# Kernel tuning notes

Hardware: AMD Instinct MI355X
Metric: run time of the kernel (lower is better)

## Reference

```python
import jax, jax.numpy as jnp
import numpy as np

BN_EPS = 1e-5


def setup_inputs() -> dict:
    key = jax.random.key(0)
    ks = jax.random.split(key, 10)
    N, C, T, V, S, IC = 128, 64, 288, 16, 3, 16
    x = jax.random.normal(ks[0], (N, C, T, V), dtype=jnp.float32)
    A_base = jax.random.uniform(ks[1], (S, V, V), dtype=jnp.float32)
    PA = jax.random.normal(ks[2], (S, V, V), dtype=jnp.float32) * 1e-3
    Wa = jax.random.normal(ks[3], (S, IC, C), dtype=jnp.float32) * 0.1
    ba = jax.random.normal(ks[4], (S, IC), dtype=jnp.float32) * 0.1
    Wb = jax.random.normal(ks[5], (S, IC, C), dtype=jnp.float32) * 0.1
    bb = jax.random.normal(ks[6], (S, IC), dtype=jnp.float32) * 0.1
    Wd = jax.random.normal(ks[7], (S, C, C), dtype=jnp.float32) * 0.1
    bd = jax.random.normal(ks[8], (S, C), dtype=jnp.float32) * 0.1
    gamma = jnp.ones((C,), dtype=jnp.float32)
    beta = jnp.zeros((C,), dtype=jnp.float32)
    return {"x": x, "A_base": A_base, "PA": PA, "Wa": Wa, "ba": ba,
            "Wb": Wb, "bb": bb, "Wd": Wd, "bd": bd,
            "gamma": gamma, "beta": beta}


def reference(x, A_base, PA, Wa, ba, Wb, bb, Wd, bd, gamma, beta):
    N, C, T, V = x.shape
    S, IC, _ = Wa.shape
    A = A_base + PA  # [s,v,w]
    # 1x1 convs for all subsets at once: [n,s,ic,t,v]
    fa = jnp.einsum('nctv,sic->nsitv', x, Wa) + ba[None, :, :, None, None]
    fb = jnp.einsum('nctv,sic->nsitv', x, Wb) + bb[None, :, :, None, None]
    # A1: permute(0,3,1,2).view(N,V,IC*T) -> [n,s,v,(ic*t)]
    A1 = fa.transpose(0, 1, 4, 2, 3).reshape(N, S, V, IC * T)
    # A2: view(N, IC*T, V) -> [n,s,(ic*t),v]
    A2 = fb.reshape(N, S, IC * T, V)
    att = jnp.einsum('nsvk,nskw->nsvw', A1, A2) / float(IC * T)
    att = jax.nn.softmax(att, axis=2)  # torch softmax(dim=1) on [N,V,V]
    att = att + A[None]  # [n,s,v,w]
    # x.view(N,C*T,V) @ att, per subset: [n,s,c,t,w]
    z = jnp.einsum('nctv,nsvw->nsctw', x, att)
    # conv_d per subset then sum over subsets
    y = jnp.einsum('nsctw,soc->notw', z, Wd) + bd.sum(0)[None, :, None, None]
    # inference BN (running mean 0, var 1)
    scale = gamma / jnp.sqrt(1.0 + BN_EPS)
    y = y * scale[None, :, None, None] + beta[None, :, None, None]
    # residual (in_channels == out_channels -> identity down path)
    return y + x
```

## Files before the change

### kernel.cpp

```cpp
#include <hip/hip_runtime.h>
#include <math.h>

#define NN 128
#define CC 64
#define TT 288
#define VV 16
#define SS 3
#define ICC 16

#define SLICES 6
#define TSL (TT / SLICES)
#define CHUNKS (TSL / 8)

typedef __attribute__((ext_vector_type(8))) short s16x8;
typedef __attribute__((ext_vector_type(4))) float f32x4;

#define MFMA16(a, b, c) __builtin_amdgcn_mfma_f32_16x16x32_bf16(a, b, c, 0, 0, 0)

__device__ __forceinline__ unsigned short f2bf(float f) {
    union { float f; unsigned u; } x; x.f = f;
    unsigned r = (x.u + 0x7FFFu + ((x.u >> 16) & 1u)) >> 16;
    return (unsigned short)r;
}

__device__ __forceinline__ unsigned cvt2bf(float lo, float hi) {
    unsigned r;
    asm("v_cvt_pk_bf16_f32 %0, %1, %2" : "=v"(r) : "v"(lo), "v"(hi));
    return r;
}

__device__ __forceinline__ s16x8 zero8() {
    s16x8 z;
#pragma unroll
    for (int j = 0; j < 8; ++j) z[j] = 0;
    return z;
}

__device__ __forceinline__ s16x8 cvt8g(const float* p) {
    float4 a = *(const float4*)p;
    float4 b = *(const float4*)(p + 4);
    union { unsigned u[4]; s16x8 v; } r;
    r.u[0] = cvt2bf(a.x, a.y); r.u[1] = cvt2bf(a.z, a.w);
    r.u[2] = cvt2bf(b.x, b.y); r.u[3] = cvt2bf(b.z, b.w);
    return r.v;
}

__global__ void k_prep(const float* __restrict__ bd, const float* __restrict__ gamma,
                       const float* __restrict__ beta, const float* __restrict__ Wd,
                       float* __restrict__ cmul, float* __restrict__ cadd,
                       unsigned short* __restrict__ wd_bf) {
    const int tid = threadIdx.x;
    if (blockIdx.x == 0 && tid < CC) {
        float mul = gamma[tid] * rsqrtf(1.0f + 1e-5f);
        float add = (bd[tid] + bd[CC + tid] + bd[2 * CC + tid]) * mul + beta[tid];
        cmul[tid] = mul;
        cadd[tid] = add;
    }
    for (int e = blockIdx.x * 256 + tid; e < SS * CC * CC; e += 16 * 256)
        wd_bf[e] = f2bf(Wd[e]);
}

__global__ __launch_bounds__(256) void k_logits(
    const float* __restrict__ x,
    const float* __restrict__ Wa, const float* __restrict__ ba,
    const float* __restrict__ Wb, const float* __restrict__ bb,
    float* __restrict__ part)
{
    const int b    = blockIdx.x;
    const int n    = b / SLICES;
    const int sl   = b % SLICES;
    const int tid  = threadIdx.x;
    const int lane = tid & 63;
    const int wave = tid >> 6;
    const int q    = lane >> 4;
    const int m    = lane & 15;

    __shared__ __align__(16) unsigned short fa_l[SS][16][136];
    __shared__ __align__(16) unsigned short fb_l[SS][16][136];
    __shared__ float red[SS][4][256];

    s16x8 wa[SS][2], wb[SS][2];
    float4 ba_r[SS], bb_r[SS];
#pragma unroll
    for (int s = 0; s < SS; ++s) {
#pragma unroll
        for (int kt = 0; kt < 2; ++kt) {
            wa[s][kt] = cvt8g(Wa + ((size_t)(s * ICC + m) * CC + kt * 32 + q * 8));
            wb[s][kt] = cvt8g(Wb + ((size_t)(s * ICC + m) * CC + kt * 32 + q * 8));
        }
        ba_r[s] = *(const float4*)(ba + s * ICC + q * 4);
        bb_r[s] = *(const float4*)(bb + s * ICC + q * 4);
    }

    f32x4 accL[SS];
#pragma unroll
    for (int s = 0; s < SS; ++s)
#pragma unroll
        for (int r = 0; r < 4; ++r) accL[s][r] = 0.0f;

    const float* xn = x + (size_t)n * CC * TT * VV;
    const int tw = sl * TSL + wave * 2;

    for (int ch = 0; ch < CHUNKS; ++ch) {
        s16x8 bx[2][2];
#pragma unroll
        for (int tli = 0; tli < 2; ++tli) {
            const float* pt = xn + (size_t)(tw + ch * 8 + tli) * VV + m;
#pragma unroll
            for (int kt = 0; kt < 2; ++kt) {
                const float* p = pt + (size_t)(kt * 32 + q * 8) * (TT * VV);
                float f0 = p[0 * TT * VV], f1 = p[1 * TT * VV];
                float f2 = p[2 * TT * VV], f3 = p[3 * TT * VV];
                float f4 = p[4 * TT * VV], f5 = p[5 * TT * VV];
                float f6 = p[6 * TT * VV], f7 = p[7 * TT * VV];
                union { unsigned u[4]; s16x8 v; } r;
                r.u[0] = cvt2bf(f0, f1); r.u[1] = cvt2bf(f2, f3);
                r.u[2] = cvt2bf(f4, f5); r.u[3] = cvt2bf(f6, f7);
                bx[tli][kt] = r.v;
            }
        }

#pragma unroll
        for (int s = 0; s < SS; ++s) {
#pragma unroll
            for (int tli = 0; tli < 2; ++tli) {
                const int tl = wave * 2 + tli;
                f32x4 aa, ab;
                aa[0] = ba_r[s].x; aa[1] = ba_r[s].y; aa[2] = ba_r[s].z; aa[3] = ba_r[s].w;
                ab[0] = bb_r[s].x; ab[1] = bb_r[s].y; ab[2] = bb_r[s].z; ab[3] = bb_r[s].w;
#pragma unroll
                for (int kt = 0; kt < 2; ++kt) {
                    aa = MFMA16(wa[s][kt], bx[tli][kt], aa);
                    ab = MFMA16(wb[s][kt], bx[tli][kt], ab);
                }
                uint2 ua, ub;
                ua.x = cvt2bf(aa[0], aa[1]); ua.y = cvt2bf(aa[2], aa[3]);
                ub.x = cvt2bf(ab[0], ab[1]); ub.y = cvt2bf(ab[2], ab[3]);
                *reinterpret_cast<uint2*>(&fa_l[s][m][tl * 16 + 4 * q]) = ua;
                *reinterpret_cast<uint2*>(&fb_l[s][m][tl * 16 + 4 * q]) = ub;
            }
            s16x8 A2 = *(const s16x8*)&fa_l[s][m][wave * 32 + q * 8];
            s16x8 B2 = *(const s16x8*)&fb_l[s][m][wave * 32 + q * 8];
            accL[s] = MFMA16(A2, B2, accL[s]);
        }
    }

    __syncthreads();
#pragma unroll
    for (int s = 0; s < SS; ++s)
#pragma unroll
        for (int r = 0; r < 4; ++r)
            red[s][wave][(4 * q + r) * 16 + m] = accL[s][r];
    __syncthreads();
#pragma unroll
    for (int s = 0; s < SS; ++s) {
        float v = red[s][0][tid & 255] + red[s][1][tid & 255] +
                  red[s][2][tid & 255] + red[s][3][tid & 255];
        part[((size_t)(sl * NN + n) * SS + s) * 256 + tid] = v;
    }
}

__global__ __launch_bounds__(256) void k_softmax(
    const float* __restrict__ part,
    const float* __restrict__ A_base, const float* __restrict__ PA,
    float* __restrict__ att)
{
    const int n = blockIdx.x / SS;
    const int s = blockIdx.x % SS;
    const int tid = threadIdx.x;
    const int w = tid & 15;

    __shared__ float l[256];
    size_t base = ((size_t)n * SS + s) * 256;
    float mine = 0.0f;
#pragma unroll
    for (int p = 0; p < SLICES; ++p)
        mine += part[(size_t)p * (NN * SS * 256) + base + tid];
    mine *= (1.0f / (ICC * TT));
    l[tid] = mine;
    __syncthreads();

    float mx = -1e30f;
#pragma unroll
    for (int v2 = 0; v2 < 16; ++v2) mx = fmaxf(mx, l[v2 * 16 + w]);
    float sm = 0.f;
#pragma unroll
    for (int v2 = 0; v2 < 16; ++v2) sm += __expf(l[v2 * 16 + w] - mx);
    float r = __expf(mine - mx) / sm;

    int aidx = (s * VV * VV) + tid;
    att[base + tid] = r + A_base[aidx] + PA[aidx];
}

__global__ __launch_bounds__(256) void k_out(
    const float* __restrict__ x, const float* __restrict__ att,
    const unsigned short* __restrict__ wd_bf,
    const float* __restrict__ cmul, const float* __restrict__ cadd,
    float* __restrict__ out)
{
    const int b  = blockIdx.x;
    const int n  = b / (TT / 8);
    const int t0 = (b % (TT / 8)) * 8;

    const int tid  = threadIdx.x;
    const int lane = tid & 63;
    const int wave = tid >> 6;
    const int q    = lane >> 4;
    const int m    = lane & 15;

    __shared__ __align__(16) unsigned short zs[4][32][72];
    __shared__ __align__(16) unsigned short attL[SS][16][24];

    for (int e = tid; e < SS * 256; e += 256) {
        int ss = e >> 8, vv = (e >> 4) & 15, ww = e & 15;
        attL[ss][ww][vv] = f2bf(att[((size_t)n * SS + ss) * 256 + vv * 16 + ww]);
    }

    s16x8 xf[4][2];
#pragma unroll
    for (int cc = 0; cc < 4; ++cc)
#pragma unroll
        for (int u = 0; u < 2; ++u) {
            s16x8 f = zero8();
            if (q < 2) {
                const float* p = x + ((size_t)(n * CC + cc * 16 + m) * TT +
                                      (t0 + wave * 2 + u)) * VV + q * 8;
                f = cvt8g(p);
            }
            xf[cc][u] = f;
        }

    __syncthreads();

    f32x4 acc[4][2];
#pragma unroll
    for (int p = 0; p < 4; ++p)
#pragma unroll
        for (int u = 0; u < 2; ++u)
#pragma unroll
            for (int r = 0; r < 4; ++r) acc[p][u][r] = 0.0f;

#pragma unroll
    for (int s = 0; s < SS; ++s) {
        s16x8 af = zero8();
        if (q < 2) af = *(const s16x8*)&attL[s][m][q * 8];

#pragma unroll
        for (int u = 0; u < 2; ++u)
#pragma unroll
            for (int cc = 0; cc < 4; ++cc) {
                f32x4 z;
#pragma unroll
                for (int r = 0; r < 4; ++r) z[r] = 0.0f;
                z = MFMA16(xf[cc][u], af, z);
                uint2 uz;
                uz.x = cvt2bf(z[0], z[1]); uz.y = cvt2bf(z[2], z[3]);
                *reinterpret_cast<uint2*>(&zs[wave][u * 16 + m][cc * 16 + 4 * q]) = uz;
            }

        s16x8 zf[2][2];
#pragma unroll
        for (int u = 0; u < 2; ++u)
#pragma unroll
            for (int kt = 0; kt < 2; ++kt)
                zf[u][kt] = *(const s16x8*)&zs[wave][u * 16 + m][kt * 32 + q * 8];

#pragma unroll
        for (int p = 0; p < 4; ++p) {
            s16x8 wf[2];
#pragma unroll
            for (int kt = 0; kt < 2; ++kt)
                wf[kt] = *(const s16x8*)(wd_bf +
                           ((size_t)(s * CC + p * 16 + m) * CC + kt * 32 + q * 8));
#pragma unroll
            for (int u = 0; u < 2; ++u)
#pragma unroll
                for (int kt = 0; kt < 2; ++kt)
                    acc[p][u] = MFMA16(wf[kt], zf[u][kt], acc[p][u]);
        }
    }

#pragma unroll
    for (int p = 0; p < 4; ++p) {
        float4 mu = *(const float4*)(cmul + p * 16 + 4 * q);
        float4 ad = *(const float4*)(cadd + p * 16 + 4 * q);
        float mur[4] = {mu.x, mu.y, mu.z, mu.w};
        float adr[4] = {ad.x, ad.y, ad.z, ad.w};
#pragma unroll
        for (int u = 0; u < 2; ++u) {
            int t = t0 + wave * 2 + u;
#pragma unroll
            for (int r = 0; r < 4; ++r) {
                int o = p * 16 + 4 * q + r;
                size_t gi = ((size_t)(n * CC + o) * TT + t) * VV + m;
                out[gi] = acc[p][u][r] * mur[r] + adr[r] + x[gi];
            }
        }
    }
}

extern "C" void kernel_launch(void* const* d_in, const int* in_sizes, int n_in,
                              void* d_out, int out_size, void* d_ws, size_t ws_size,
                              hipStream_t stream) {
    const float* x      = (const float*)d_in[0];
    const float* A_base = (const float*)d_in[1];
    const float* PA     = (const float*)d_in[2];
    const float* Wa     = (const float*)d_in[3];
    const float* ba     = (const float*)d_in[4];
    const float* Wb     = (const float*)d_in[5];
    const float* bb     = (const float*)d_in[6];
    const float* Wd     = (const float*)d_in[7];
    const float* bd     = (const float*)d_in[8];
    const float* gamma  = (const float*)d_in[9];
    const float* beta   = (const float*)d_in[10];
    float* out = (float*)d_out;

    float* part = (float*)d_ws;
    float* att  = part;
    float* cmul = part + (size_t)SLICES * NN * SS * 256;
    float* cadd = cmul + CC;
    unsigned short* wd_bf = (unsigned short*)(cadd + CC);

    k_prep<<<16, 256, 0, stream>>>(bd, gamma, beta, Wd, cmul, cadd, wd_bf);
    k_logits<<<NN * SLICES, 256, 0, stream>>>(x, Wa, ba, Wb, bb, part);
    k_softmax<<<NN * SS, 256, 0, stream>>>(part, A_base, PA, att);
    k_out<<<NN * (TT / 8), 256, 0, stream>>>(x, att, wd_bf, cmul, cadd, out);
}
```

Baseline: 417.4 us.

## Stage x and Wd through swizzled LDS with coalesced loads and stores

In the logits kernel, x is loaded as coalesced float4 rows into a register prefetch buffer, converted to bf16 and written to an XOR-swizzled LDS tile. MFMA fragments are then read from that tile, replacing the per-lane strided gathers, and the next chunk is prefetched while the current one computes. The time slices per sample double. The output kernel now handles 16 timesteps per block. It stages x and the bf16 Wd weights in swizzled LDS and routes results through LDS so the residual add and stores use coalesced float4 accesses. This raises LDS use and adds barriers in exchange for fewer uncoalesced global transactions.

After: 340.9 us. 1.22x faster.

```diff
diff --git a/kernel.cpp b/kernel.cpp
--- a/kernel.cpp
+++ b/kernel.cpp
@@ -8,9 +8,11 @@
 #define SS 3
 #define ICC 16
 
-#define SLICES 6
+#define SLICES 12
 #define TSL (TT / SLICES)
 #define CHUNKS (TSL / 8)
+
+#define OTB 16
 
 typedef __attribute__((ext_vector_type(8))) short s16x8;
 typedef __attribute__((ext_vector_type(4))) float f32x4;
@@ -43,6 +45,15 @@
     r.u[0] = cvt2bf(a.x, a.y); r.u[1] = cvt2bf(a.z, a.w);
     r.u[2] = cvt2bf(b.x, b.y); r.u[3] = cvt2bf(b.z, b.w);
     return r.v;
+}
+
+__device__ __forceinline__ int xaddr(int col, int c) {
+    int chunk = ((c >> 3) ^ (col & 7) ^ ((col >> 3) & 7)) & 7;
+    return col * 64 + chunk * 8 + (c & 7);
+}
+__device__ __forceinline__ int xaddr16(int col, int ck) {
+    int chunk = (ck ^ (col & 7) ^ ((col >> 3) & 7)) & 7;
+    return col * 64 + chunk * 8;
 }
 
 __global__ void k_prep(const float* __restrict__ bd, const float* __restrict__ gamma,
@@ -75,9 +86,9 @@
     const int q    = lane >> 4;
     const int m    = lane & 15;
 
+    __shared__ __align__(16) unsigned short xsb[128 * 64];
     __shared__ __align__(16) unsigned short fa_l[SS][16][136];
     __shared__ __align__(16) unsigned short fb_l[SS][16][136];
-    __shared__ float red[SS][4][256];
 
     s16x8 wa[SS][2], wb[SS][2];
     float4 ba_r[SS], bb_r[SS];
@@ -99,24 +110,48 @@
         for (int r = 0; r < 4; ++r) accL[s][r] = 0.0f;
 
     const float* xn = x + (size_t)n * CC * TT * VV;
-    const int tw = sl * TSL + wave * 2;
-
+    const int tbase = sl * TSL;
+
+    float4 px[8];
+#pragma unroll
+    for (int i = 0; i < 8; ++i) {
+        int f4 = tid + i * 256;
+        int c = f4 >> 5, col4 = (f4 & 31) * 4;
+        px[i] = *(const float4*)(xn + (size_t)c * (TT * VV) + (size_t)tbase * VV + col4);
+    }
+
+#pragma unroll
     for (int ch = 0; ch < CHUNKS; ++ch) {
+        __syncthreads();
+#pragma unroll
+        for (int i = 0; i < 8; ++i) {
+            int f4 = tid + i * 256;
+            int c = f4 >> 5, col4 = (f4 & 31) * 4;
+            unsigned s01 = cvt2bf(px[i].x, px[i].y);
+            unsigned s23 = cvt2bf(px[i].z, px[i].w);
+            xsb[xaddr(col4 + 0, c)] = (unsigned short)(s01 & 0xffff);
+            xsb[xaddr(col4 + 1, c)] = (unsigned short)(s01 >> 16);
+            xsb[xaddr(col4 + 2, c)] = (unsigned short)(s23 & 0xffff);
+            xsb[xaddr(col4 + 3, c)] = (unsigned short)(s23 >> 16);
+        }
+        __syncthreads();
+
         s16x8 bx[2][2];
 #pragma unroll
         for (int tli = 0; tli < 2; ++tli) {
-            const float* pt = xn + (size_t)(tw + ch * 8 + tli) * VV + m;
-#pragma unroll
-            for (int kt = 0; kt < 2; ++kt) {
-                const float* p = pt + (size_t)(kt * 32 + q * 8) * (TT * VV);
-                float f0 = p[0 * TT * VV], f1 = p[1 * TT * VV];
-                float f2 = p[2 * TT * VV], f3 = p[3 * TT * VV];
-                float f4 = p[4 * TT * VV], f5 = p[5 * TT * VV];
-                float f6 = p[6 * TT * VV], f7 = p[7 * TT * VV];
-                union { unsigned u[4]; s16x8 v; } r;
-                r.u[0] = cvt2bf(f0, f1); r.u[1] = cvt2bf(f2, f3);
-                r.u[2] = cvt2bf(f4, f5); r.u[3] = cvt2bf(f6, f7);
-                bx[tli][kt] = r.v;
+            int col = (wave * 2 + tli) * 16 + m;
+#pragma unroll
+            for (int kt = 0; kt < 2; ++kt)
+                bx[tli][kt] = *(const s16x8*)&xsb[xaddr16(col, kt * 4 + q)];
+        }
+
+        if (ch + 1 < CHUNKS) {
+#pragma unroll
+            for (int i = 0; i < 8; ++i) {
+                int f4 = tid + i * 256;
+                int c = f4 >> 5, col4 = (f4 & 31) * 4;
+                px[i] = *(const float4*)(xn + (size_t)c * (TT * VV) +
+                                         (size_t)(tbase + (ch + 1) * 8) * VV + col4);
             }
         }
 
@@ -146,16 +181,17 @@
     }
 
     __syncthreads();
+    float* red = (float*)xsb;
 #pragma unroll
     for (int s = 0; s < SS; ++s)
 #pragma unroll
         for (int r = 0; r < 4; ++r)
-            red[s][wave][(4 * q + r) * 16 + m] = accL[s][r];
+            red[(s * 4 + wave) * 256 + (4 * q + r) * 16 + m] = accL[s][r];
     __syncthreads();
 #pragma unroll
     for (int s = 0; s < SS; ++s) {
-        float v = red[s][0][tid & 255] + red[s][1][tid & 255] +
-                  red[s][2][tid & 255] + red[s][3][tid & 255];
+        float v = red[(s * 4 + 0) * 256 + tid] + red[(s * 4 + 1) * 256 + tid] +
+                  red[(s * 4 + 2) * 256 + tid] + red[(s * 4 + 3) * 256 + tid];
         part[((size_t)(sl * NN + n) * SS + s) * 256 + tid] = v;
     }
 }
@@ -199,8 +235,8 @@
     float* __restrict__ out)
 {
     const int b  = blockIdx.x;
-    const int n  = b / (TT / 8);
-    const int t0 = (b % (TT / 8)) * 8;
+    const int n  = b / (TT / OTB);
+    const int t0 = (b % (TT / OTB)) * OTB;
 
     const int tid  = threadIdx.x;
     const int lane = tid & 63;
@@ -208,35 +244,64 @@
     const int q    = lane >> 4;
     const int m    = lane & 15;
 
-    __shared__ __align__(16) unsigned short zs[4][32][72];
+    __shared__ __align__(16) unsigned char uni[36864];
+    __shared__ __align__(16) unsigned short wdl[SS * 64 * 64];
     __shared__ __align__(16) unsigned short attL[SS][16][24];
 
+    unsigned short* xsb = (unsigned short*)uni;
+    unsigned short* zsb = (unsigned short*)uni;
+    float*          osb = (float*)uni;
+
+    {
+        const float* xrow0 = x + ((size_t)(n * CC) * TT + t0) * VV;
+#pragma unroll
+        for (int i = 0; i < 16; ++i) {
+            int c = wave * 16 + i;
+            float4 f = *(const float4*)(xrow0 + (size_t)c * (TT * VV) + lane * 4);
+            uint2 u2; u2.x = cvt2bf(f.x, f.y); u2.y = cvt2bf(f.z, f.w);
+            int tcol  = lane * 4;
+            int chunk = (tcol >> 3) ^ (c & 7);
+            *(uint2*)&xsb[c * 256 + chunk * 8 + (tcol & 7)] = u2;
+        }
+    }
+#pragma unroll
+    for (int i = 0; i < 12; ++i) {
+        int g  = tid + i * 256;
+        int s  = g >> 10;
+        int r1 = g & 1023;
+        int o  = r1 >> 4, c4 = r1 & 15;
+        uint2 w2 = *(const uint2*)(wd_bf + ((size_t)(s * 64 + o) * 64 + c4 * 4));
+        int chunk = (c4 >> 1) ^ (o & 7);
+        *(uint2*)&wdl[(s * 64 + o) * 64 + chunk * 8 + (c4 & 1) * 4] = w2;
+    }
     for (int e = tid; e < SS * 256; e += 256) {
         int ss = e >> 8, vv = (e >> 4) & 15, ww = e & 15;
         attL[ss][ww][vv] = f2bf(att[((size_t)n * SS + ss) * 256 + vv * 16 + ww]);
     }
 
-    s16x8 xf[4][2];
+    __syncthreads();
+
+    s16x8 xf[4][4];
 #pragma unroll
     for (int cc = 0; cc < 4; ++cc)
 #pragma unroll
-        for (int u = 0; u < 2; ++u) {
+        for (int u = 0; u < 4; ++u) {
             s16x8 f = zero8();
             if (q < 2) {
-                const float* p = x + ((size_t)(n * CC + cc * 16 + m) * TT +
-                                      (t0 + wave * 2 + u)) * VV + q * 8;
-                f = cvt8g(p);
+                int c = cc * 16 + m;
+                int chunk = ((4 * wave + u) * 2 + q) ^ (c & 7);
+                f = *(const s16x8*)&xsb[c * 256 + chunk * 8];
             }
             xf[cc][u] = f;
         }
 
     __syncthreads();
 
-    f32x4 acc[4][2];
+    f32x4 acc[4][4];
 #pragma unroll
     for (int p = 0; p < 4; ++p)
 #pragma unroll
-        for (int u = 0; u < 2; ++u)
+        for (int u = 0; u < 4; ++u)
 #pragma unroll
             for (int r = 0; r < 4; ++r) acc[p][u][r] = 0.0f;
 
@@ -246,34 +311,36 @@
         if (q < 2) af = *(const s16x8*)&attL[s][m][q * 8];
 
 #pragma unroll
-        for (int u = 0; u < 2; ++u)
+        for (int u = 0; u < 4; ++u)
 #pragma unroll
             for (int cc = 0; cc < 4; ++cc) {
                 f32x4 z;
 #pragma unroll
                 for (int r = 0; r < 4; ++r) z[r] = 0.0f;
                 z = MFMA16(xf[cc][u], af, z);
-                uint2 uz;
-                uz.x = cvt2bf(z[0], z[1]); uz.y = cvt2bf(z[2], z[3]);
-                *reinterpret_cast<uint2*>(&zs[wave][u * 16 + m][cc * 16 + 4 * q]) = uz;
+                uint2 uz; uz.x = cvt2bf(z[0], z[1]); uz.y = cvt2bf(z[2], z[3]);
+                *(uint2*)&zsb[((wave * 64) + u * 16 + m) * 72 + cc * 16 + 4 * q] = uz;
             }
 
-        s16x8 zf[2][2];
-#pragma unroll
-        for (int u = 0; u < 2; ++u)
+        s16x8 zf[4][2];
+#pragma unroll
+        for (int u = 0; u < 4; ++u)
 #pragma unroll
             for (int kt = 0; kt < 2; ++kt)
-                zf[u][kt] = *(const s16x8*)&zs[wave][u * 16 + m][kt * 32 + q * 8];
+                zf[u][kt] = *(const s16x8*)&zsb[((wave * 64) + u * 16 + m) * 72 +
+                                                kt * 32 + q * 8];
 
 #pragma unroll
         for (int p = 0; p < 4; ++p) {
             s16x8 wf[2];
 #pragma unroll
-            for (int kt = 0; kt < 2; ++kt)
-                wf[kt] = *(const s16x8*)(wd_bf +
-                           ((size_t)(s * CC + p * 16 + m) * CC + kt * 32 + q * 8));
-#pragma unroll
-            for (int u = 0; u < 2; ++u)
+            for (int kt = 0; kt < 2; ++kt) {
+                int o = p * 16 + m;
+                int chunk = (kt * 4 + q) ^ (o & 7);
+                wf[kt] = *(const s16x8*)&wdl[(s * 64 + o) * 64 + chunk * 8];
+            }
+#pragma unroll
+            for (int u = 0; u < 4; ++u)
 #pragma unroll
                 for (int kt = 0; kt < 2; ++kt)
                     acc[p][u] = MFMA16(wf[kt], zf[u][kt], acc[p][u]);
@@ -287,14 +354,35 @@
         float mur[4] = {mu.x, mu.y, mu.z, mu.w};
         float adr[4] = {ad.x, ad.y, ad.z, ad.w};
 #pragma unroll
-        for (int u = 0; u < 2; ++u) {
-            int t = t0 + wave * 2 + u;
-#pragma unroll
-            for (int r = 0; r < 4; ++r) {
-                int o = p * 16 + 4 * q + r;
-                size_t gi = ((size_t)(n * CC + o) * TT + t) * VV + m;
-                out[gi] = acc[p][u][r] * mur[r] + adr[r] + x[gi];
-            }
+        for (int u = 0; u < 4; ++u)
+#pragma unroll
+            for (int r = 0; r < 4; ++r)
+                acc[p][u][r] = acc[p][u][r] * mur[r] + adr[r];
+    }
+
+#pragma unroll
+    for (int hp = 0; hp < 2; ++hp) {
+        __syncthreads();
+#pragma unroll
+        for (int pp = 0; pp < 2; ++pp)
+#pragma unroll
+            for (int u = 0; u < 4; ++u)
+#pragma unroll
+                for (int r = 0; r < 4; ++r)
+                    osb[(pp * 16 + 4 * q + r) * 268 + (4 * wave + u) * 16 + m] =
+                        acc[hp * 2 + pp][u][r];
+        __syncthreads();
+#pragma unroll
+        for (int j = 0; j < 8; ++j) {
+            int orow = wave * 8 + j;
+            int o = hp * 32 + orow;
+            float4 v = *(const float4*)&osb[orow * 268 + lane * 4];
+            size_t off = ((size_t)(n * CC + o) * TT + t0) * VV + lane * 4;
+            float4 xr = *(const float4*)(x + off);
+            float4 res;
+            res.x = v.x + xr.x; res.y = v.y + xr.y;
+            res.z = v.z + xr.z; res.w = v.w + xr.w;
+            *(float4*)(out + off) = res;
         }
     }
 }
@@ -324,5 +412,5 @@
     k_prep<<<16, 256, 0, stream>>>(bd, gamma, beta, Wd, cmul, cadd, wd_bf);
     k_logits<<<NN * SLICES, 256, 0, stream>>>(x, Wa, ba, Wb, bb, part);
     k_softmax<<<NN * SS, 256, 0, stream>>>(part, A_base, PA, att);
-    k_out<<<NN * (TT / 8), 256, 0, stream>>>(x, att, wd_bf, cmul, cadd, out);
-}
+    k_out<<<NN * (TT / OTB), 256, 0, stream>>>(x, att, wd_bf, cmul, cadd, out);
+}
```
